# Kernel optimization log

Measured on AMD Instinct MI355X. Metric: run time of the kernel, lower is better.

The kernel has to match this reference:

```python
import jax, jax.numpy as jnp
import numpy as np
import math

B, S, D, H = 2, 2048, 2048, 16
DH = D // H
SCALE = math.sqrt(DH)


def setup_inputs() -> dict:
    key = jax.random.key(0)
    ks = jax.random.split(key, 9)
    x = jax.random.normal(ks[0], (B, S, D), dtype=jnp.float32)
    # causal mask: True above the diagonal -> masked (matches masked_fill(mask, -inf))
    mask = jnp.triu(jnp.ones((S, S), dtype=jnp.bool_), k=1)
    std = 0.02
    wq = jax.random.normal(ks[1], (D, D), jnp.float32) * std
    wk = jax.random.normal(ks[2], (D, D), jnp.float32) * std
    wv = jax.random.normal(ks[3], (D, D), jnp.float32) * std
    wo = jax.random.normal(ks[4], (D, D), jnp.float32) * std
    bq = jnp.zeros((D,), jnp.float32)
    bk = jnp.zeros((D,), jnp.float32)
    bv = jnp.zeros((D,), jnp.float32)
    bo = jnp.zeros((D,), jnp.float32)
    return {"x": x, "mask": mask, "wq": wq, "bq": bq, "wk": wk, "bk": bk,
            "wv": wv, "bv": bv, "wo": wo, "bo": bo}


def reference(x, mask, wq, bq, wk, bk, wv, bv, wo, bo):
    b, s, d = x.shape
    # projections (nn.Linear: y = x @ W^T + b)
    q = (x @ wq.T + bq).reshape(b, s, H, DH).transpose(0, 2, 1, 3)  # [b,h,s,dh]
    k = (x @ wk.T + bk).reshape(b, s, H, DH).transpose(0, 2, 1, 3)
    v = (x @ wv.T + bv).reshape(b, s, H, DH).transpose(0, 2, 1, 3)
    scores = jnp.einsum('bhqd,bhkd->bhqk', q, k) / SCALE
    scores = jnp.where(mask[None, None, :, :], -jnp.inf, scores)
    attn = jax.nn.softmax(scores, axis=-1)
    out = jnp.einsum('bhqk,bhkd->bhqd', attn, v)  # [b,h,s,dh]
    out = out.transpose(0, 2, 1, 3).reshape(b, s, d)
    return out @ wo.T + bo
```

## Files before the change

### kernel.cpp

```cpp
#include <hip/hip_runtime.h>
#include <hip/hip_bf16.h>


using u16 = unsigned short;
typedef float  f32x4  __attribute__((ext_vector_type(4)));
typedef short  short8 __attribute__((ext_vector_type(8)));

#define DEV __device__ __forceinline__

constexpr int Bc = 2, Sc = 2048, Dc = 2048, Hc = 16, DHc = 128, Mc = 4096, Kc = 2048;
constexpr float RSCALE = 0.08838834764831845f;
constexpr float L2E    = 1.44269504088896341f;

DEV u16 f2bf(float f) { __bf16 h = (__bf16)f; return __builtin_bit_cast(u16, h); }

DEV void gload_lds16(const void* gsrc, void* lds) {
  __builtin_amdgcn_global_load_lds(
      (const __attribute__((address_space(1))) unsigned int*)gsrc,
      (__attribute__((address_space(3))) unsigned int*)lds, 16, 0, 0);
}

__global__ void cast_all(const float* __restrict__ x, const float* __restrict__ wq,
                         const float* __restrict__ wk, const float* __restrict__ wv,
                         const float* __restrict__ wo, u16* __restrict__ XB,
                         u16* __restrict__ WQKV, u16* __restrict__ WOb) {
  const int i = blockIdx.x * blockDim.x + threadIdx.x;
  const float4* src;
  u16* dst;
  if (i < 2097152)      { src = (const float4*)x  + i;             dst = XB   + (size_t)i * 4; }
  else if (i < 3145728) { src = (const float4*)wq + (i - 2097152); dst = WQKV + (size_t)(i - 2097152) * 4; }
  else if (i < 4194304) { src = (const float4*)wk + (i - 3145728); dst = WQKV + 4194304 + (size_t)(i - 3145728) * 4; }
  else if (i < 5242880) { src = (const float4*)wv + (i - 4194304); dst = WQKV + 8388608 + (size_t)(i - 4194304) * 4; }
  else                  { src = (const float4*)wo + (i - 5242880); dst = WOb  + (size_t)(i - 5242880) * 4; }
  float4 v = *src;
  u16 o0 = f2bf(v.x), o1 = f2bf(v.y), o2 = f2bf(v.z), o3 = f2bf(v.w);
  dst[0] = o0; dst[1] = o1; dst[2] = o2; dst[3] = o3;
}

template <int BN, int FR, int EPI>
__global__ __launch_bounds__(512, 2) void gemm2p(
    const u16* __restrict__ A, const u16* __restrict__ W,
    const float* __restrict__ bias0, const float* __restrict__ bias1,
    const float* __restrict__ bias2,
    u16* __restrict__ q_out, u16* __restrict__ k_out, u16* __restrict__ vt_out,
    float* __restrict__ f_out) {
  constexpr int LB = BN / 64;
  constexpr int NWR = (EPI == 0) ? 6144 : 2048;
  constexpr int NBX = NWR / BN, NBY = Mc / 256, TOT = NBX * NBY, PX = TOT / 8;
  constexpr int NT = Kc / 64;
  static_assert(BN == FR * 64, "8 waves: 4 N-cols x 16*FR");

  __shared__ u16 lsA[2][256 * 64];
  __shared__ u16 lsB[2][BN * 64];

  const int tid = threadIdx.x;
  const int lane = tid & 63;
  const int w = tid >> 6;
  const int wr = w >> 2, wc = w & 3;
  const int l15 = lane & 15, l4 = lane >> 4;

  const int id = blockIdx.x;
  const int wg = (id & 7) * PX + (id >> 3);
  const int bx = wg / NBY, by = wg % NBY;
  const int m0 = by * 256, n0 = bx * BN;

  const int srow = tid >> 3;
  const int spc = tid & 7;
  const int slc = spc ^ (srow & 7);

  auto stA = [&](int buf, int t, int j) {
    gload_lds16(A + (size_t)(m0 + j * 64 + srow) * Kc + t * 64 + slc * 8,
                &lsA[buf][j * 4096 + tid * 8]);
  };
  auto stB = [&](int buf, int t, int j) {
    gload_lds16(W + (size_t)(n0 + j * 64 + srow) * Kc + t * 64 + slc * 8,
                &lsB[buf][j * 4096 + tid * 8]);
  };

  const int pc0 = l4 ^ (l15 & 7);
  const int pc1 = (4 + l4) ^ (l15 & 7);

  f32x4 acc[8][FR] = {};
  short8 af[8], bf[FR * 2];

  auto ldA = [&](int buf, int half) {
#pragma unroll
    for (int fm = 0; fm < 4; ++fm) {
      const u16* base = &lsA[buf][(wr * 128 + half * 64 + fm * 16 + l15) * 64];
      af[fm * 2 + 0] = *(const short8*)(base + pc0 * 8);
      af[fm * 2 + 1] = *(const short8*)(base + pc1 * 8);
    }
  };
  auto ldB = [&](int buf) {
#pragma unroll
    for (int f = 0; f < FR; ++f) {
      const u16* base = &lsB[buf][(wc * (16 * FR) + f * 16 + l15) * 64];
      bf[f * 2 + 0] = *(const short8*)(base + pc0 * 8);
      bf[f * 2 + 1] = *(const short8*)(base + pc1 * 8);
    }
  };
  auto mma = [&](int half) {
#pragma unroll
    for (int ks = 0; ks < 2; ++ks)
#pragma unroll
      for (int fm = 0; fm < 4; ++fm)
#pragma unroll
        for (int f = 0; f < FR; ++f)
          acc[half * 4 + fm][f] = __builtin_amdgcn_mfma_f32_16x16x32_bf16(
              af[fm * 2 + ks], bf[f * 2 + ks], acc[half * 4 + fm][f], 0, 0, 0);
  };

#pragma unroll
  for (int j = 0; j < LB; ++j) stB(0, 0, j);
  stA(0, 0, 0); stA(0, 0, 2);
  stA(0, 0, 1); stA(0, 0, 3);
  asm volatile("s_waitcnt vmcnt(2)" ::: "memory");
  __builtin_amdgcn_s_barrier();

#pragma unroll 1
  for (int u = 0; u < NT; ++u) {
    const int c = u & 1;
    ldA(c, 0);
    ldB(c);
    if (u + 1 < NT) {
#pragma unroll
      for (int j = 0; j < LB; ++j) stB(c ^ 1, u + 1, j);
      stA(c ^ 1, u + 1, 0); stA(c ^ 1, u + 1, 2);
    }
    __builtin_amdgcn_s_barrier();
    asm volatile("s_waitcnt lgkmcnt(0)" ::: "memory");
    __builtin_amdgcn_s_setprio(1); mma(0); __builtin_amdgcn_s_setprio(0);
    if (u + 1 < NT) {
      if constexpr (LB == 3) asm volatile("s_waitcnt vmcnt(5)" ::: "memory");
      else                   asm volatile("s_waitcnt vmcnt(4)" ::: "memory");
    } else {
      asm volatile("s_waitcnt vmcnt(0)" ::: "memory");
    }
    __builtin_amdgcn_s_barrier();
    ldA(c, 1);
    if (u + 1 < NT) { stA(c ^ 1, u + 1, 1); stA(c ^ 1, u + 1, 3); }
    __builtin_amdgcn_s_barrier();
    asm volatile("s_waitcnt lgkmcnt(0)" ::: "memory");
    __builtin_amdgcn_s_setprio(1); mma(1); __builtin_amdgcn_s_setprio(0);
    if (u + 1 < NT) asm volatile("s_waitcnt vmcnt(2)" ::: "memory");
    __builtin_amdgcn_s_barrier();
  }

  if constexpr (EPI == 0) {
#pragma unroll
    for (int f = 0; f < FR; ++f) {
      const int n = n0 + wc * (16 * FR) + f * 16 + l15;
      const int sec = n >> 11;
      const int n2 = n & 2047;
      const float bias = sec == 0 ? bias0[n2] : (sec == 1 ? bias1[n2] : bias2[n2]);
      const int h = n2 >> 7, dh = n2 & 127;
#pragma unroll
      for (int fm = 0; fm < 8; ++fm) {
        const int m = m0 + wr * 128 + fm * 16 + l4 * 4;
        const int bb = m >> 11, s = m & 2047;
        if (sec < 2) {
          const float scl = sec == 0 ? RSCALE : 1.0f;
          u16* dst = sec == 0 ? q_out : k_out;
#pragma unroll
          for (int r = 0; r < 4; ++r)
            dst[((size_t)(bb * Hc + h) * Sc + s + r) * DHc + dh] =
                f2bf((acc[fm][f][r] + bias) * scl);
        } else {
          ushort4 pk;
          pk.x = f2bf(acc[fm][f][0] + bias);
          pk.y = f2bf(acc[fm][f][1] + bias);
          pk.z = f2bf(acc[fm][f][2] + bias);
          pk.w = f2bf(acc[fm][f][3] + bias);
          *(ushort4*)&vt_out[((size_t)(bb * Hc + h) * DHc + dh) * Sc + s] = pk;
        }
      }
    }
  } else {
#pragma unroll
    for (int f = 0; f < FR; ++f) {
      const int n = n0 + wc * (16 * FR) + f * 16 + l15;
      const float bias = bias0[n];
#pragma unroll
      for (int fm = 0; fm < 8; ++fm) {
        const int m = m0 + wr * 128 + fm * 16 + l4 * 4;
#pragma unroll
        for (int r = 0; r < 4; ++r)
          f_out[(size_t)(m + r) * Dc + n] = acc[fm][f][r] + bias;
      }
    }
  }
}

__global__ __launch_bounds__(256) void fattn(
    const u16* __restrict__ Qb, const u16* __restrict__ Kb,
    const u16* __restrict__ VTb, u16* __restrict__ AO) {
  __shared__ u16 lsK[2][64 * 128];
  __shared__ u16 lsV[2][128 * 64];
  __shared__ u16 lsP[4][16 * 64];

  const int tid = threadIdx.x;
  const int lane = tid & 63;
  const int w = tid >> 6;
  const int l15 = lane & 15, l4 = lane >> 4;

  const int id = blockIdx.x;
  const int xcd = id & 7, seq = id >> 3;
  const int bh = xcd + 8 * (seq >> 4);
  const int pair = seq & 15;

  const int b = bh >> 4, h = bh & 15;
  const size_t kbase = (size_t)bh * Sc * DHc;
  const size_t vbase = (size_t)bh * DHc * Sc;

#pragma unroll 1
  for (int qsel = 0; qsel < 2; ++qsel) {
    const int qt = qsel ? (31 - pair) : pair;
    const int q0 = qt * 64;
    const int ntiles = qt + 1;

    const size_t qbase = ((size_t)bh * Sc + q0 + w * 16 + l15) * DHc;
    short8 qf[4];
#pragma unroll
    for (int ks = 0; ks < 4; ++ks)
      qf[ks] = *(const short8*)&Qb[qbase + ks * 32 + l4 * 8];

    float m_run[4], l_run[4];
#pragma unroll
    for (int r = 0; r < 4; ++r) { m_run[r] = -__builtin_inff(); l_run[r] = 0.f; }
    f32x4 o_acc[8] = {};

    auto stageKV = [&](int sb, int ti) {
      const int kv0 = ti * 64;
#pragma unroll
      for (int c = 0; c < 4; ++c) {
        int p = c * 256 + tid;
        int row = p >> 4, ph = p & 15;
        int lg = (ph & 8) | ((ph ^ row) & 7);
        gload_lds16(Kb + kbase + (size_t)(kv0 + row) * DHc + lg * 8, &lsK[sb][p * 8]);
      }
#pragma unroll
      for (int c = 0; c < 4; ++c) {
        int p = c * 256 + tid;
        int row = p >> 3, ph = p & 7;
        int lg = ph ^ (row & 7);
        gload_lds16(VTb + vbase + (size_t)row * Sc + kv0 + lg * 8, &lsV[sb][p * 8]);
      }
    };

    stageKV(0, 0);
    asm volatile("s_waitcnt vmcnt(0)" ::: "memory");
    __syncthreads();

    int buf = 0;
#pragma unroll 1
    for (int ti = 0; ti < ntiles; ++ti) {
      const int kv0 = ti * 64;
      if (ti + 1 < ntiles) stageKV(buf ^ 1, ti + 1);

      f32x4 s[4] = {};
      __builtin_amdgcn_s_setprio(1);
#pragma unroll
      for (int nf = 0; nf < 4; ++nf) {
        int row = nf * 16 + l15;
#pragma unroll
        for (int ks = 0; ks < 4; ++ks) {
          int lg = ks * 4 + l4;
          int pc = (lg & 8) | ((lg ^ row) & 7);
          short8 kf = *(const short8*)&lsK[buf][row * 128 + pc * 8];
          s[nf] = __builtin_amdgcn_mfma_f32_16x16x32_bf16(qf[ks], kf, s[nf], 0, 0, 0);
        }
      }
      __builtin_amdgcn_s_setprio(0);

      if (kv0 == q0) {
#pragma unroll
        for (int nf = 0; nf < 4; ++nf) {
          int kc = nf * 16 + l15;
#pragma unroll
          for (int r = 0; r < 4; ++r)
            if (kc > w * 16 + l4 * 4 + r) s[nf][r] = -__builtin_inff();
        }
      }
      float alpha[4];
#pragma unroll
      for (int r = 0; r < 4; ++r) {
        float mx = fmaxf(fmaxf(s[0][r], s[1][r]), fmaxf(s[2][r], s[3][r]));
        mx = fmaxf(mx, __shfl_xor(mx, 1));
        mx = fmaxf(mx, __shfl_xor(mx, 2));
        mx = fmaxf(mx, __shfl_xor(mx, 4));
        mx = fmaxf(mx, __shfl_xor(mx, 8));
        float mnew = fmaxf(m_run[r], mx);
        alpha[r] = __builtin_amdgcn_exp2f((m_run[r] - mnew) * L2E);
        m_run[r] = mnew;
      }
#pragma unroll
      for (int nf = 0; nf < 4; ++nf)
#pragma unroll
        for (int r = 0; r < 4; ++r)
          s[nf][r] = __builtin_amdgcn_exp2f((s[nf][r] - m_run[r]) * L2E);
#pragma unroll
      for (int r = 0; r < 4; ++r) {
        float sm = s[0][r] + s[1][r] + s[2][r] + s[3][r];
        sm += __shfl_xor(sm, 1);
        sm += __shfl_xor(sm, 2);
        sm += __shfl_xor(sm, 4);
        sm += __shfl_xor(sm, 8);
        l_run[r] = l_run[r] * alpha[r] + sm;
      }
#pragma unroll
      for (int nf2 = 0; nf2 < 8; ++nf2)
#pragma unroll
        for (int r = 0; r < 4; ++r) o_acc[nf2][r] *= alpha[r];

#pragma unroll
      for (int nf = 0; nf < 4; ++nf)
#pragma unroll
        for (int r = 0; r < 4; ++r) {
          int rif = l4 * 4 + r;
          int kc = nf * 16 + l15;
          int pc = (kc >> 3) ^ (rif & 7);
          lsP[w][rif * 64 + pc * 8 + (kc & 7)] = f2bf(s[nf][r]);
        }
      asm volatile("s_waitcnt lgkmcnt(0)" ::: "memory");

      __builtin_amdgcn_s_setprio(1);
#pragma unroll
      for (int ks = 0; ks < 2; ++ks) {
        int pc = (ks * 4 + l4) ^ (l15 & 7);
        short8 pa = *(const short8*)&lsP[w][l15 * 64 + pc * 8];
#pragma unroll
        for (int nf2 = 0; nf2 < 8; ++nf2) {
          int vrow = nf2 * 16 + l15;
          int vpc = (ks * 4 + l4) ^ (vrow & 7);
          short8 vb = *(const short8*)&lsV[buf][vrow * 64 + vpc * 8];
          o_acc[nf2] = __builtin_amdgcn_mfma_f32_16x16x32_bf16(pa, vb, o_acc[nf2], 0, 0, 0);
        }
      }
      __builtin_amdgcn_s_setprio(0);

      asm volatile("s_waitcnt vmcnt(0)" ::: "memory");
      __syncthreads();
      buf ^= 1;
    }

#pragma unroll
    for (int nf2 = 0; nf2 < 8; ++nf2)
#pragma unroll
      for (int r = 0; r < 4; ++r) {
        int qr = q0 + w * 16 + l4 * 4 + r;
        float ov = o_acc[nf2][r] / l_run[r];
        AO[((size_t)(b * Sc + qr)) * Dc + h * DHc + nf2 * 16 + l15] = f2bf(ov);
      }
    __syncthreads();
  }
}

extern "C" void kernel_launch(void* const* d_in, const int* in_sizes, int n_in,
                              void* d_out, int out_size, void* d_ws, size_t ws_size,
                              hipStream_t stream) {
  const float* x  = (const float*)d_in[0];
  const float* wq = (const float*)d_in[2];
  const float* bq = (const float*)d_in[3];
  const float* wk = (const float*)d_in[4];
  const float* bk = (const float*)d_in[5];
  const float* wv = (const float*)d_in[6];
  const float* bv = (const float*)d_in[7];
  const float* wo = (const float*)d_in[8];
  const float* bo = (const float*)d_in[9];
  float* out = (float*)d_out;

  char* ws = (char*)d_ws;
  u16* WQKV = (u16*)(ws + 0);
  u16* WOb  = (u16*)(ws + 25165824);
  u16* XB   = (u16*)(ws + 33554432);
  u16* Qb   = (u16*)(ws + 50331648);
  u16* Kb   = (u16*)(ws + 67108864);
  u16* VTb  = (u16*)(ws + 100663296);
  u16* AO   = XB;

  cast_all<<<dim3(24576), dim3(256), 0, stream>>>(x, wq, wk, wv, wo, XB, WQKV, WOb);
  gemm2p<192, 3, 0><<<dim3(512), dim3(512), 0, stream>>>(
      XB, WQKV, bq, bk, bv, Qb, Kb, VTb, nullptr);
  fattn<<<dim3(512), dim3(256), 0, stream>>>(Qb, Kb, VTb, AO);
  gemm2p<128, 2, 1><<<dim3(256), dim3(512), 0, stream>>>(
      AO, WOb, bo, nullptr, nullptr, nullptr, nullptr, nullptr, out);
}
```

Baseline: 397.1 us.

## Software-pipeline GEMM main loop with register double-buffered LDS fragments and deeper prefetch

Restructures the bf16 MFMA GEMM main loop so the LDS fragment reads for the next K-tile (B fragments and the first A half) are issued before the current tile's second MFMA half. Global-to-LDS prefetch is now two tiles ahead instead of one. The loop is unrolled by two so B fragments can ping-pong between two register arrays. Partial lgkmcnt waits and sched_barriers replace full drains, aiming to overlap LDS latency and global loads with MFMA work and to cut one barrier per half-step. The cost is more VGPR pressure, which may lower occupancy or cause spills. The hand-counted waitcnt values are fragile, and the unroll by two assumes NT is even.

```diff
diff --git a/kernel.cpp b/kernel.cpp
--- a/kernel.cpp
+++ b/kernel.cpp
@@ -81,17 +81,25 @@
   const int pc1 = (4 + l4) ^ (l15 & 7);
 
   f32x4 acc[8][FR] = {};
-  short8 af[8], bf[FR * 2];
-
-  auto ldA = [&](int buf, int half) {
+  short8 aH0[8], aH1[8], bA[FR * 2], bB[FR * 2];
+
+  auto rdA0 = [&](int buf) {
 #pragma unroll
     for (int fm = 0; fm < 4; ++fm) {
-      const u16* base = &lsA[buf][(wr * 128 + half * 64 + fm * 16 + l15) * 64];
-      af[fm * 2 + 0] = *(const short8*)(base + pc0 * 8);
-      af[fm * 2 + 1] = *(const short8*)(base + pc1 * 8);
-    }
-  };
-  auto ldB = [&](int buf) {
+      const u16* base = &lsA[buf][(wr * 128 + fm * 16 + l15) * 64];
+      aH0[fm * 2 + 0] = *(const short8*)(base + pc0 * 8);
+      aH0[fm * 2 + 1] = *(const short8*)(base + pc1 * 8);
+    }
+  };
+  auto rdA1 = [&](int buf) {
+#pragma unroll
+    for (int fm = 0; fm < 4; ++fm) {
+      const u16* base = &lsA[buf][(wr * 128 + 64 + fm * 16 + l15) * 64];
+      aH1[fm * 2 + 0] = *(const short8*)(base + pc0 * 8);
+      aH1[fm * 2 + 1] = *(const short8*)(base + pc1 * 8);
+    }
+  };
+  auto rdB = [&](int buf, short8* bf) {
 #pragma unroll
     for (int f = 0; f < FR; ++f) {
       const u16* base = &lsB[buf][(wc * (16 * FR) + f * 16 + l15) * 64];
@@ -99,7 +107,7 @@
       bf[f * 2 + 1] = *(const short8*)(base + pc1 * 8);
     }
   };
-  auto mma = [&](int half) {
+  auto mma = [&](const short8* af, const short8* bf, int half) {
 #pragma unroll
     for (int ks = 0; ks < 2; ++ks)
 #pragma unroll
@@ -114,36 +122,50 @@
   for (int j = 0; j < LB; ++j) stB(0, 0, j);
   stA(0, 0, 0); stA(0, 0, 2);
   stA(0, 0, 1); stA(0, 0, 3);
-  asm volatile("s_waitcnt vmcnt(2)" ::: "memory");
+#pragma unroll
+  for (int j = 0; j < LB; ++j) stB(1, 1, j);
+  stA(1, 1, 0); stA(1, 1, 2);
+  if constexpr (LB == 3) asm volatile("s_waitcnt vmcnt(5)" ::: "memory");
+  else                   asm volatile("s_waitcnt vmcnt(4)" ::: "memory");
   __builtin_amdgcn_s_barrier();
-
-#pragma unroll 1
-  for (int u = 0; u < NT; ++u) {
-    const int c = u & 1;
-    ldA(c, 0);
-    ldB(c);
+  rdB(0, bA);
+  rdA0(0);
+
+  auto body = [&](int u, int c, short8* bCur, short8* bNxt) {
+    rdA1(c);
+    if (u + 1 < NT) { stA(c ^ 1, u + 1, 1); stA(c ^ 1, u + 1, 3); }
+    asm volatile("s_waitcnt lgkmcnt(8)" ::: "memory");
+    __builtin_amdgcn_sched_barrier(0);
+    __builtin_amdgcn_s_setprio(1); mma(aH0, bCur, 0); __builtin_amdgcn_s_setprio(0);
+    if (u + 1 < NT) asm volatile("s_waitcnt vmcnt(2)" ::: "memory");
+    __builtin_amdgcn_s_barrier();
+    if (u + 1 < NT) { rdB(c ^ 1, bNxt); rdA0(c ^ 1); }
+    if (u + 2 < NT) {
+#pragma unroll
+      for (int j = 0; j < LB; ++j) stB(c, u + 2, j);
+      stA(c, u + 2, 0); stA(c, u + 2, 2);
+    }
     if (u + 1 < NT) {
-#pragma unroll
-      for (int j = 0; j < LB; ++j) stB(c ^ 1, u + 1, j);
-      stA(c ^ 1, u + 1, 0); stA(c ^ 1, u + 1, 2);
-    }
-    __builtin_amdgcn_s_barrier();
-    asm volatile("s_waitcnt lgkmcnt(0)" ::: "memory");
-    __builtin_amdgcn_s_setprio(1); mma(0); __builtin_amdgcn_s_setprio(0);
-    if (u + 1 < NT) {
+      if constexpr (FR == 3) asm volatile("s_waitcnt lgkmcnt(14)" ::: "memory");
+      else                   asm volatile("s_waitcnt lgkmcnt(12)" ::: "memory");
+    } else {
+      asm volatile("s_waitcnt lgkmcnt(0)" ::: "memory");
+    }
+    __builtin_amdgcn_sched_barrier(0);
+    __builtin_amdgcn_s_setprio(1); mma(aH1, bCur, 1); __builtin_amdgcn_s_setprio(0);
+    if (u + 2 < NT) {
       if constexpr (LB == 3) asm volatile("s_waitcnt vmcnt(5)" ::: "memory");
       else                   asm volatile("s_waitcnt vmcnt(4)" ::: "memory");
-    } else {
+    } else if (u + 1 < NT) {
       asm volatile("s_waitcnt vmcnt(0)" ::: "memory");
     }
     __builtin_amdgcn_s_barrier();
-    ldA(c, 1);
-    if (u + 1 < NT) { stA(c ^ 1, u + 1, 1); stA(c ^ 1, u + 1, 3); }
-    __builtin_amdgcn_s_barrier();
-    asm volatile("s_waitcnt lgkmcnt(0)" ::: "memory");
-    __builtin_amdgcn_s_setprio(1); mma(1); __builtin_amdgcn_s_setprio(0);
-    if (u + 1 < NT) asm volatile("s_waitcnt vmcnt(2)" ::: "memory");
-    __builtin_amdgcn_s_barrier();
+  };
+
+#pragma unroll 1
+  for (int u = 0; u < NT; u += 2) {
+    body(u, 0, bA, bB);
+    body(u + 1, 1, bB, bA);
   }
 
   if constexpr (EPI == 0) {
```

Result: slower. 509.9 us (+28.4%).
